# Performance work log

Measured on AMD Instinct MI355X. Metric: run time of the kernel, lower is better.

The kernel has to match this reference:

```python
import jax, jax.numpy as jnp
import numpy as np

N_HEADS = 32
N_KV_HEADS = 8
HEAD_DIM = 64
ROPE_THETA = 10000.0
NEG_INF = -1e9


def apply_rope(t, offset=0):
    # t: [B, H, L, hd]; half-split (rotate-half) RoPE convention
    B, H, L, hd = t.shape
    pos = jnp.arange(offset, offset + L, dtype=jnp.float32)            # [L]
    inv_freq = 1.0 / (ROPE_THETA ** (jnp.arange(0, hd, 2, dtype=jnp.float32) / hd))  # [hd/2]
    ang = pos[:, None] * inv_freq[None, :]                              # [L, hd/2]
    cos = jnp.cos(ang).astype(t.dtype)
    sin = jnp.sin(ang).astype(t.dtype)
    t1, t2 = jnp.split(t, 2, axis=-1)                                   # each [B,H,L,hd/2]
    return jnp.concatenate([t1 * cos - t2 * sin, t1 * sin + t2 * cos], axis=-1)


def setup_inputs() -> dict:
    key = jax.random.key(0)
    ks = jax.random.split(key, 6)
    B, L, D = 1, 2048, 2048
    x = jax.random.normal(ks[0], (B, L, D), dtype=jnp.float32)
    attn_scale = jnp.ones((1,), dtype=jnp.float32)
    # causal additive mask: 0 on/below diagonal, -1e9 above
    mask = jnp.where(jnp.tril(jnp.ones((L, L), dtype=bool)), 0.0, NEG_INF).astype(jnp.float32)
    s = 0.02
    Wq = jax.random.normal(ks[1], (N_HEADS * HEAD_DIM, D), dtype=jnp.float32) * s
    Wk = jax.random.normal(ks[2], (N_KV_HEADS * HEAD_DIM, D), dtype=jnp.float32) * s
    Wv = jax.random.normal(ks[3], (N_KV_HEADS * HEAD_DIM, D), dtype=jnp.float32) * s
    Wo = jax.random.normal(ks[4], (D, N_HEADS * HEAD_DIM), dtype=jnp.float32) * s
    return {"x": x, "attn_scale": attn_scale, "mask": mask,
            "Wq": Wq, "Wk": Wk, "Wv": Wv, "Wo": Wo}


def reference(x, attn_scale, mask, Wq, Wk, Wv, Wo):
    B, L, D = x.shape
    scale = HEAD_DIM ** -0.5
    # projections (nn.Linear: y = x @ W.T)
    q = (x @ Wq.T).reshape(B, L, N_HEADS, HEAD_DIM).transpose(0, 2, 1, 3)     # [B,H,L,hd]
    k = (x @ Wk.T).reshape(B, L, N_KV_HEADS, HEAD_DIM).transpose(0, 2, 1, 3)  # [B,Hk,L,hd]
    v = (x @ Wv.T).reshape(B, L, N_KV_HEADS, HEAD_DIM).transpose(0, 2, 1, 3)
    q = apply_rope(q)
    k = apply_rope(k)
    q = q * attn_scale  # elementwise attn_scale applied to queries
    # GQA: repeat kv heads
    rep = N_HEADS // N_KV_HEADS
    k = jnp.repeat(k, rep, axis=1)
    v = jnp.repeat(v, rep, axis=1)
    scores = jnp.einsum('bhld,bhmd->bhlm', q, k) * scale + mask
    probs = jax.nn.softmax(scores, axis=-1)
    out = jnp.einsum('bhlm,bhmd->bhld', probs, v)          # [B,H,L,hd]
    out = out.transpose(0, 2, 1, 3).reshape(B, L, N_HEADS * HEAD_DIM)
    return out @ Wo.T
```

## Files before the change

kernel.cpp:

```cpp
#include <hip/hip_runtime.h>
#include <stdint.h>

typedef short bf16x8 __attribute__((ext_vector_type(8)));
typedef float f32x4 __attribute__((ext_vector_type(4)));

__device__ __forceinline__ unsigned short f2bf(float f) {
  uint32_t u = __float_as_uint(f);
  u = (u + 0x7FFFu + ((u >> 16) & 1u)) >> 16;
  return (unsigned short)u;
}

__device__ __forceinline__ void gload16(const void* g, void* lds) {
  const __attribute__((address_space(1))) char* gp =
      (const __attribute__((address_space(1))) char*)(uintptr_t)g;
  __attribute__((address_space(3))) char* sp =
      (__attribute__((address_space(3))) char*)(uint32_t)(uintptr_t)lds;
  __builtin_amdgcn_global_load_lds(gp, sp, 16, 0, 0);
}

__global__ void k_cvt_all(const float* __restrict__ x, const float* __restrict__ Wq,
                          const float* __restrict__ Wk, const float* __restrict__ Wv,
                          const float* __restrict__ Wo, unsigned short* __restrict__ xb,
                          unsigned short* __restrict__ Wcat, unsigned short* __restrict__ Wob) {
  int b = blockIdx.x;
  const float* src;
  unsigned short* dst;
  int off;
  if (b < 4096)       { src = x;  dst = xb;                  off = b; }
  else if (b < 8192)  { src = Wq; dst = Wcat;                off = b - 4096; }
  else if (b < 9216)  { src = Wk; dst = Wcat + 2048 * 2048;  off = b - 8192; }
  else if (b < 10240) { src = Wv; dst = Wcat + 2560 * 2048;  off = b - 9216; }
  else                { src = Wo; dst = Wob;                  off = b - 10240; }
  int i = off * 256 + threadIdx.x;
  float4 v = ((const float4*)src)[i];
  ushort4 o;
  o.x = f2bf(v.x); o.y = f2bf(v.y); o.z = f2bf(v.z); o.w = f2bf(v.w);
  ((ushort4*)dst)[i] = o;
}

template <int OUTF32, int ROPE>
__global__ __launch_bounds__(256) void k_gemm(const unsigned short* __restrict__ A,
                                              const unsigned short* __restrict__ B,
                                              void* __restrict__ Cout,
                                              int M, int N, int K,
                                              const float* __restrict__ scale_p,
                                              unsigned short* __restrict__ vtout) {
  __shared__ unsigned short As[2][64 * 64];
  __shared__ unsigned short Bs[2][128 * 64];
  const int tid = threadIdx.x;
  const int w = tid >> 6, lane = tid & 63;
  const int g = lane >> 4, cl = lane & 15;
  const int nTn = N >> 7;
  const int per = gridDim.x >> 3;
  const int bid = (blockIdx.x & 7) * per + (blockIdx.x >> 3);
  const int tm = bid / nTn, tn = bid % nTn;
  const int m0 = tm << 6, n0 = tn << 7;
  const int wm = (w >> 1) << 5, wn = (w & 1) << 6;
  f32x4 acc[2][4] = {};

  auto stage = [&](int kt, int b) {
#pragma unroll
    for (int it = 0; it < 6; ++it) {
      int cc = tid + it * 256;
      int isB = cc >= 512;
      int c3 = isB ? (cc - 512) : cc;
      int row = c3 >> 3, kb = (c3 & 7) << 4;
      const unsigned short* base = isB ? (B + (size_t)(n0 + row) * K + kt)
                                       : (A + (size_t)(m0 + row) * K + kt);
      const char* src = (const char*)base + (kb ^ ((row & 7) << 4));
      char* dstl = (char*)(isB ? Bs[b] : As[b]) + c3 * 16;
      gload16(src, dstl);
    }
  };

  stage(0, 0);
  asm volatile("s_waitcnt vmcnt(0)" ::: "memory");
  __syncthreads();
  int buf = 0;

  for (int kt = 0; kt < K; kt += 64) {
    if (kt + 64 < K) stage(kt + 64, buf ^ 1);
#pragma unroll
    for (int ks = 0; ks < 2; ++ks) {
      bf16x8 af[2], bfr[4];
#pragma unroll
      for (int i = 0; i < 2; ++i) {
        int row = wm + i * 16 + cl;
        int kb = ((g << 4) + (ks << 6)) ^ ((row & 7) << 4);
        af[i] = *(const bf16x8*)((const char*)As[buf] + row * 128 + kb);
      }
#pragma unroll
      for (int j = 0; j < 4; ++j) {
        int row = wn + j * 16 + cl;
        int kb = ((g << 4) + (ks << 6)) ^ ((row & 7) << 4);
        bfr[j] = *(const bf16x8*)((const char*)Bs[buf] + row * 128 + kb);
      }
#pragma unroll
      for (int i = 0; i < 2; ++i)
#pragma unroll
        for (int j = 0; j < 4; ++j)
          acc[i][j] = __builtin_amdgcn_mfma_f32_16x16x32_bf16(af[i], bfr[j], acc[i][j], 0, 0, 0);
    }
    asm volatile("s_waitcnt vmcnt(0)" ::: "memory");
    __syncthreads();
    buf ^= 1;
  }

  if (ROPE && n0 >= 2560) {
#pragma unroll
    for (int i = 0; i < 2; ++i)
#pragma unroll
      for (int j = 0; j < 4; ++j) {
        int d = n0 - 2560 + wn + j * 16 + cl;
        int l0r = m0 + wm + i * 16 + (g << 2);
        ushort4 o;
        o.x = f2bf(acc[i][j][0]); o.y = f2bf(acc[i][j][1]);
        o.z = f2bf(acc[i][j][2]); o.w = f2bf(acc[i][j][3]);
        *(ushort4*)(vtout + (size_t)d * 2048 + l0r) = o;
      }
    return;
  }

  if (ROPE) {
    float s0v = scale_p[0] * 0.125f * 1.4426950408889634f;
    float sc = (n0 < 2048) ? s0v : 1.0f;
    float invf[2];
#pragma unroll
    for (int j = 0; j < 2; ++j)
      invf[j] = __expf(-(float)(j * 16 + cl) * 0.2878231366242557f);
#pragma unroll
    for (int i = 0; i < 2; ++i)
#pragma unroll
      for (int r = 0; r < 4; ++r) {
        float pos = (float)(m0 + wm + i * 16 + (g << 2) + r);
#pragma unroll
        for (int j = 0; j < 2; ++j) {
          float ang = pos * invf[j];
          float sn, cs;
          __sincosf(ang, &sn, &cs);
          float t1 = acc[i][j][r], t2 = acc[i][j + 2][r];
          acc[i][j][r] = (t1 * cs - t2 * sn) * sc;
          acc[i][j + 2][r] = (t1 * sn + t2 * cs) * sc;
        }
      }
  }

#pragma unroll
  for (int i = 0; i < 2; ++i)
#pragma unroll
    for (int j = 0; j < 4; ++j)
#pragma unroll
      for (int r = 0; r < 4; ++r) {
        int row = m0 + wm + i * 16 + (g << 2) + r;
        int col = n0 + wn + j * 16 + cl;
        float v = acc[i][j][r];
        if (OUTF32)
          ((float*)Cout)[(size_t)row * N + col] = v;
        else
          ((unsigned short*)Cout)[(size_t)row * N + col] = f2bf(v);
      }
}

__global__ __launch_bounds__(256) void k_attn(const unsigned short* __restrict__ qkv,
                                              const unsigned short* __restrict__ vt,
                                              unsigned short* __restrict__ ao) {
  __shared__ unsigned short Ks[2][64 * 64];
  __shared__ unsigned short Vs[2][64 * 64];
  __shared__ unsigned short Ps[4 * 16 * 64];
  const int tid = threadIdx.x;
  const int w = tid >> 6, lane = tid & 63;
  const int g = lane >> 4, cl = lane & 15;
  const int h = blockIdx.x & 31;
  const int qb = 31 - (blockIdx.x >> 5);
  const int q0 = qb << 6;
  const int hk = h >> 2;
  const int qg = q0 + w * 16 + cl;

  const unsigned short* qptr = qkv + (size_t)qg * 3072 + h * 64 + g * 8;
  bf16x8 qf0 = *(const bf16x8*)qptr;
  bf16x8 qf1 = *(const bf16x8*)(qptr + 32);

  const short ob = (short)0x3F80;
  const bf16x8 onesf = {ob, ob, ob, ob, ob, ob, ob, ob};

  f32x4 acc[4] = {};
  f32x4 acc_l = {};

  char* myP = (char*)Ps + w * 2048;

  int kvOff[2][4];
#pragma unroll
  for (int ks = 0; ks < 2; ++ks)
#pragma unroll
    for (int t = 0; t < 4; ++t) {
      int row = t * 16 + cl;
      kvOff[ks][t] = row * 128 + (((g << 4) + (ks << 6)) ^ ((row & 7) << 4));
    }
  int pwOff[4];
#pragma unroll
  for (int t = 0; t < 4; ++t)
    pwOff[t] = cl * 128 + (((t << 5) + (g << 3)) ^ ((cl & 7) << 4));
  int prOff[2];
#pragma unroll
  for (int ks = 0; ks < 2; ++ks)
    prOff[ks] = cl * 128 + (((g << 4) + (ks << 6)) ^ ((cl & 7) << 4));

  const int row0 = tid >> 3, row1 = (tid + 256) >> 3;
  const int kb0 = (tid & 7) << 4, kb1 = ((tid + 256) & 7) << 4;
  const char* kSrc0 = (const char*)(qkv + 2048 + hk * 64 + (size_t)row0 * 3072) + (kb0 ^ ((row0 & 7) << 4));
  const char* kSrc1 = (const char*)(qkv + 2048 + hk * 64 + (size_t)row1 * 3072) + (kb1 ^ ((row1 & 7) << 4));
  const char* vSrc0 = (const char*)(vt + (size_t)hk * 64 * 2048 + (size_t)row0 * 2048) + (kb0 ^ ((row0 & 7) << 4));
  const char* vSrc1 = (const char*)(vt + (size_t)hk * 64 * 2048 + (size_t)row1 * 2048) + (kb1 ^ ((row1 & 7) << 4));

  auto stageK = [&](int ck, int b) {
    size_t off = (size_t)ck * 393216;
    gload16(kSrc0 + off, (char*)Ks[b] + tid * 16);
    gload16(kSrc1 + off, (char*)Ks[b] + (tid + 256) * 16);
  };
  auto stageV = [&](int ck, int b) {
    size_t off = (size_t)ck * 128;
    gload16(vSrc0 + off, (char*)Vs[b] + tid * 16);
    gload16(vSrc1 + off, (char*)Vs[b] + (tid + 256) * 16);
  };

  stageK(0, 0); stageV(0, 0);
  if (qb >= 1) stageK(1, 1);
  asm volatile("s_waitcnt vmcnt(0)" ::: "memory");
  __syncthreads();

  float svA[4][4], svB[4][4];
  {
    const char* Kc = (const char*)Ks[0];
    __builtin_amdgcn_s_setprio(1);
#pragma unroll
    for (int t = 0; t < 4; ++t) {
      f32x4 stv = {};
#pragma unroll
      for (int ks = 0; ks < 2; ++ks) {
        bf16x8 kf = *(const bf16x8*)(Kc + kvOff[ks][t]);
        stv = __builtin_amdgcn_mfma_f32_16x16x32_bf16(kf, ks ? qf1 : qf0, stv, 0, 0, 0);
      }
#pragma unroll
      for (int r = 0; r < 4; ++r) svA[t][r] = stv[r];
    }
    __builtin_amdgcn_s_setprio(0);
  }
  __syncthreads();

#define ATTN_BODY(I, CUR, NXT)                                                         \
  {                                                                                    \
    const int i_ = (I);                                                                \
    if (i_ + 2 <= qb) stageK(i_ + 2, i_ & 1);                                          \
    if (i_ + 1 <= qb) stageV(i_ + 1, (i_ + 1) & 1);                                    \
    if (i_ < qb) {                                                                     \
      const char* Kc = (const char*)Ks[(i_ + 1) & 1];                                  \
      __builtin_amdgcn_s_setprio(1);                                                   \
      _Pragma("unroll")                                                                \
      for (int t = 0; t < 4; ++t) {                                                    \
        f32x4 stv = {};                                                                \
        _Pragma("unroll")                                                              \
        for (int ks = 0; ks < 2; ++ks) {                                               \
          bf16x8 kf = *(const bf16x8*)(Kc + kvOff[ks][t]);                             \
          stv = __builtin_amdgcn_mfma_f32_16x16x32_bf16(kf, ks ? qf1 : qf0, stv, 0, 0, 0); \
        }                                                                              \
        _Pragma("unroll")                                                              \
        for (int r = 0; r < 4; ++r) NXT[t][r] = stv[r];                                \
      }                                                                                \
      __builtin_amdgcn_s_setprio(0);                                                   \
    }                                                                                  \
    if (i_ == qb) {                                                                    \
      const int kv0 = i_ << 6;                                                         \
      _Pragma("unroll")                                                                \
      for (int t = 0; t < 4; ++t)                                                      \
        _Pragma("unroll")                                                              \
        for (int r = 0; r < 4; ++r) {                                                  \
          int kvg = kv0 + t * 16 + (g << 2) + r;                                       \
          if (kvg > qg) CUR[t][r] = -1e9f;                                             \
        }                                                                              \
    }                                                                                  \
    _Pragma("unroll")                                                                  \
    for (int t = 0; t < 4; ++t) {                                                      \
      float e0 = __builtin_exp2f(CUR[t][0]);                                           \
      float e1 = __builtin_exp2f(CUR[t][1]);                                           \
      float e2 = __builtin_exp2f(CUR[t][2]);                                           \
      float e3 = __builtin_exp2f(CUR[t][3]);                                           \
      uint32_t d0, d1;                                                                 \
      asm("v_cvt_pk_bf16_f32 %0, %1, %2" : "=v"(d0) : "v"(e0), "v"(e1));               \
      asm("v_cvt_pk_bf16_f32 %0, %1, %2" : "=v"(d1) : "v"(e2), "v"(e3));               \
      uint2 dd; dd.x = d0; dd.y = d1;                                                  \
      *(uint2*)(myP + pwOff[t]) = dd;                                                  \
    }                                                                                  \
    {                                                                                  \
      const char* Vc = (const char*)Vs[i_ & 1];                                        \
      __builtin_amdgcn_s_setprio(1);                                                   \
      _Pragma("unroll")                                                                \
      for (int ks = 0; ks < 2; ++ks) {                                                 \
        bf16x8 pf = *(const bf16x8*)(myP + prOff[ks]);                                 \
        acc_l = __builtin_amdgcn_mfma_f32_16x16x32_bf16(pf, onesf, acc_l, 0, 0, 0);    \
        _Pragma("unroll")                                                              \
        for (int t = 0; t < 4; ++t) {                                                  \
          bf16x8 vf = *(const bf16x8*)(Vc + kvOff[ks][t]);                             \
          acc[t] = __builtin_amdgcn_mfma_f32_16x16x32_bf16(pf, vf, acc[t], 0, 0, 0);   \
        }                                                                              \
      }                                                                                \
      __builtin_amdgcn_s_setprio(0);                                                   \
    }                                                                                  \
    if (i_ < qb) {                                                                     \
      asm volatile("s_waitcnt vmcnt(0)" ::: "memory");                                 \
      __syncthreads();                                                                 \
    }                                                                                  \
  }

  for (int i = 0; i <= qb; i += 2) {
    ATTN_BODY(i, svA, svB);
    if (i + 1 <= qb) ATTN_BODY(i + 1, svB, svA);
  }
#undef ATTN_BODY

  float li[4];
#pragma unroll
  for (int r = 0; r < 4; ++r) li[r] = 1.0f / acc_l[r];
#pragma unroll
  for (int t = 0; t < 4; ++t)
#pragma unroll
    for (int r = 0; r < 4; ++r) {
      int row = q0 + w * 16 + (g << 2) + r;
      int col = h * 64 + t * 16 + cl;
      ao[(size_t)row * 2048 + col] = f2bf(acc[t][r] * li[r]);
    }
}

extern "C" void kernel_launch(void* const* d_in, const int* in_sizes, int n_in,
                              void* d_out, int out_size, void* d_ws, size_t ws_size,
                              hipStream_t stream) {
  (void)in_sizes; (void)n_in; (void)out_size; (void)ws_size;
  const float* x  = (const float*)d_in[0];
  const float* sc = (const float*)d_in[1];
  const float* Wq = (const float*)d_in[3];
  const float* Wk = (const float*)d_in[4];
  const float* Wv = (const float*)d_in[5];
  const float* Wo = (const float*)d_in[6];
  float* out = (float*)d_out;
  char* ws = (char*)d_ws;
  unsigned short* xb   = (unsigned short*)(ws);
  unsigned short* Wcat = (unsigned short*)(ws + 8388608);
  unsigned short* Wob  = (unsigned short*)(ws + 20971520);
  unsigned short* QKV  = (unsigned short*)(ws + 29360128);
  unsigned short* VT   = (unsigned short*)(ws + 41943040);
  unsigned short* AO   = (unsigned short*)(ws + 44040192);

  k_cvt_all<<<14336, 256, 0, stream>>>(x, Wq, Wk, Wv, Wo, xb, Wcat, Wob);
  k_gemm<0, 1><<<768, 256, 0, stream>>>(xb, Wcat, QKV, 2048, 3072, 2048, sc, VT);
  k_attn<<<1024, 256, 0, stream>>>(QKV, VT, AO);
  k_gemm<1, 0><<<512, 256, 0, stream>>>(AO, Wob, out, 2048, 2048, 2048, nullptr, nullptr);
}
```

Measured before the change: 116.1 us.

## Fuse attention and output projection into one persistent launch with per-row-block counters

The attention kernel and the output-projection GEMM are merged into one launch of 1536 blocks. Output-GEMM blocks spin on per-query-block completion counters, so each row tile starts once all 32 heads for that row block are written, overlapping the projection with the attention tail. The output GEMM also changes from the K=64 tiling to a K=32 tiling with its own swizzle. This saves a kernel launch and the tail idle time, at the cost of a memset, spin-waiting blocks that hold CU slots, and a deadlock risk if GEMM blocks get scheduled before attention blocks finish.

```diff
diff --git a/kernel.cpp b/kernel.cpp
--- a/kernel.cpp
+++ b/kernel.cpp
@@ -38,13 +38,12 @@
   ((ushort4*)dst)[i] = o;
 }
 
-template <int OUTF32, int ROPE>
-__global__ __launch_bounds__(256) void k_gemm(const unsigned short* __restrict__ A,
-                                              const unsigned short* __restrict__ B,
-                                              void* __restrict__ Cout,
-                                              int M, int N, int K,
-                                              const float* __restrict__ scale_p,
-                                              unsigned short* __restrict__ vtout) {
+__global__ __launch_bounds__(256) void k_gemm0(const unsigned short* __restrict__ A,
+                                               const unsigned short* __restrict__ B,
+                                               unsigned short* __restrict__ Cout,
+                                               const float* __restrict__ scale_p,
+                                               unsigned short* __restrict__ vtout) {
+  const int K = 2048, N = 3072;
   __shared__ unsigned short As[2][64 * 64];
   __shared__ unsigned short Bs[2][128 * 64];
   const int tid = threadIdx.x;
@@ -106,7 +105,7 @@
     buf ^= 1;
   }
 
-  if (ROPE && n0 >= 2560) {
+  if (n0 >= 2560) {
 #pragma unroll
     for (int i = 0; i < 2; ++i)
 #pragma unroll
@@ -121,7 +120,7 @@
     return;
   }
 
-  if (ROPE) {
+  {
     float s0v = scale_p[0] * 0.125f * 1.4426950408889634f;
     float sc = (n0 < 2048) ? s0v : 1.0f;
     float invf[2];
@@ -153,181 +152,257 @@
       for (int r = 0; r < 4; ++r) {
         int row = m0 + wm + i * 16 + (g << 2) + r;
         int col = n0 + wn + j * 16 + cl;
-        float v = acc[i][j][r];
-        if (OUTF32)
-          ((float*)Cout)[(size_t)row * N + col] = v;
-        else
-          ((unsigned short*)Cout)[(size_t)row * N + col] = f2bf(v);
-      }
-}
-
-__global__ __launch_bounds__(256) void k_attn(const unsigned short* __restrict__ qkv,
-                                              const unsigned short* __restrict__ vt,
-                                              unsigned short* __restrict__ ao) {
-  __shared__ unsigned short Ks[2][64 * 64];
-  __shared__ unsigned short Vs[2][64 * 64];
-  __shared__ unsigned short Ps[4 * 16 * 64];
+        Cout[(size_t)row * N + col] = f2bf(acc[i][j][r]);
+      }
+}
+
+__global__ __launch_bounds__(256) void k_attn_g1(const unsigned short* __restrict__ qkv,
+                                                 const unsigned short* __restrict__ vt,
+                                                 unsigned short* __restrict__ ao,
+                                                 const unsigned short* __restrict__ Wob,
+                                                 float* __restrict__ out,
+                                                 int* __restrict__ done) {
+  __shared__ __align__(16) char smem[40960];
   const int tid = threadIdx.x;
   const int w = tid >> 6, lane = tid & 63;
   const int g = lane >> 4, cl = lane & 15;
-  const int h = blockIdx.x & 31;
-  const int qb = 31 - (blockIdx.x >> 5);
-  const int q0 = qb << 6;
-  const int hk = h >> 2;
-  const int qg = q0 + w * 16 + cl;
-
-  const unsigned short* qptr = qkv + (size_t)qg * 3072 + h * 64 + g * 8;
-  bf16x8 qf0 = *(const bf16x8*)qptr;
-  bf16x8 qf1 = *(const bf16x8*)(qptr + 32);
-
-  const short ob = (short)0x3F80;
-  const bf16x8 onesf = {ob, ob, ob, ob, ob, ob, ob, ob};
-
-  f32x4 acc[4] = {};
-  f32x4 acc_l = {};
-
-  char* myP = (char*)Ps + w * 2048;
-
-  int kvOff[2][4];
-#pragma unroll
-  for (int ks = 0; ks < 2; ++ks)
-#pragma unroll
-    for (int t = 0; t < 4; ++t) {
-      int row = t * 16 + cl;
-      kvOff[ks][t] = row * 128 + (((g << 4) + (ks << 6)) ^ ((row & 7) << 4));
-    }
-  int pwOff[4];
-#pragma unroll
-  for (int t = 0; t < 4; ++t)
-    pwOff[t] = cl * 128 + (((t << 5) + (g << 3)) ^ ((cl & 7) << 4));
-  int prOff[2];
-#pragma unroll
-  for (int ks = 0; ks < 2; ++ks)
-    prOff[ks] = cl * 128 + (((g << 4) + (ks << 6)) ^ ((cl & 7) << 4));
-
-  const int row0 = tid >> 3, row1 = (tid + 256) >> 3;
-  const int kb0 = (tid & 7) << 4, kb1 = ((tid + 256) & 7) << 4;
-  const char* kSrc0 = (const char*)(qkv + 2048 + hk * 64 + (size_t)row0 * 3072) + (kb0 ^ ((row0 & 7) << 4));
-  const char* kSrc1 = (const char*)(qkv + 2048 + hk * 64 + (size_t)row1 * 3072) + (kb1 ^ ((row1 & 7) << 4));
-  const char* vSrc0 = (const char*)(vt + (size_t)hk * 64 * 2048 + (size_t)row0 * 2048) + (kb0 ^ ((row0 & 7) << 4));
-  const char* vSrc1 = (const char*)(vt + (size_t)hk * 64 * 2048 + (size_t)row1 * 2048) + (kb1 ^ ((row1 & 7) << 4));
-
-  auto stageK = [&](int ck, int b) {
-    size_t off = (size_t)ck * 393216;
-    gload16(kSrc0 + off, (char*)Ks[b] + tid * 16);
-    gload16(kSrc1 + off, (char*)Ks[b] + (tid + 256) * 16);
-  };
-  auto stageV = [&](int ck, int b) {
-    size_t off = (size_t)ck * 128;
-    gload16(vSrc0 + off, (char*)Vs[b] + tid * 16);
-    gload16(vSrc1 + off, (char*)Vs[b] + (tid + 256) * 16);
-  };
-
-  stageK(0, 0); stageV(0, 0);
-  if (qb >= 1) stageK(1, 1);
-  asm volatile("s_waitcnt vmcnt(0)" ::: "memory");
-  __syncthreads();
-
-  float svA[4][4], svB[4][4];
-  {
-    const char* Kc = (const char*)Ks[0];
-    __builtin_amdgcn_s_setprio(1);
-#pragma unroll
-    for (int t = 0; t < 4; ++t) {
-      f32x4 stv = {};
-#pragma unroll
-      for (int ks = 0; ks < 2; ++ks) {
-        bf16x8 kf = *(const bf16x8*)(Kc + kvOff[ks][t]);
-        stv = __builtin_amdgcn_mfma_f32_16x16x32_bf16(kf, ks ? qf1 : qf0, stv, 0, 0, 0);
-      }
-#pragma unroll
-      for (int r = 0; r < 4; ++r) svA[t][r] = stv[r];
-    }
-    __builtin_amdgcn_s_setprio(0);
-  }
-  __syncthreads();
+
+  if (blockIdx.x < 1024) {
+    unsigned short (*Ks)[64 * 64] = (unsigned short (*)[64 * 64])smem;
+    unsigned short (*Vs)[64 * 64] = (unsigned short (*)[64 * 64])(smem + 16384);
+    char* Ps = smem + 32768;
+    const int h = blockIdx.x & 31;
+    const int qb = 31 - (blockIdx.x >> 5);
+    const int q0 = qb << 6;
+    const int hk = h >> 2;
+    const int qg = q0 + w * 16 + cl;
+
+    const unsigned short* qptr = qkv + (size_t)qg * 3072 + h * 64 + g * 8;
+    bf16x8 qf0 = *(const bf16x8*)qptr;
+    bf16x8 qf1 = *(const bf16x8*)(qptr + 32);
+
+    const short ob = (short)0x3F80;
+    const bf16x8 onesf = {ob, ob, ob, ob, ob, ob, ob, ob};
+
+    f32x4 acc[4] = {};
+    f32x4 acc_l = {};
+
+    char* myP = Ps + w * 2048;
+
+    int kvOff[2][4];
+#pragma unroll
+    for (int ks = 0; ks < 2; ++ks)
+#pragma unroll
+      for (int t = 0; t < 4; ++t) {
+        int row = t * 16 + cl;
+        kvOff[ks][t] = row * 128 + (((g << 4) + (ks << 6)) ^ ((row & 7) << 4));
+      }
+    int pwOff[4];
+#pragma unroll
+    for (int t = 0; t < 4; ++t)
+      pwOff[t] = cl * 128 + (((t << 5) + (g << 3)) ^ ((cl & 7) << 4));
+    int prOff[2];
+#pragma unroll
+    for (int ks = 0; ks < 2; ++ks)
+      prOff[ks] = cl * 128 + (((g << 4) + (ks << 6)) ^ ((cl & 7) << 4));
+
+    const int row0 = tid >> 3, row1 = (tid + 256) >> 3;
+    const int kb0 = (tid & 7) << 4, kb1 = ((tid + 256) & 7) << 4;
+    const char* kSrc0 = (const char*)(qkv + 2048 + hk * 64 + (size_t)row0 * 3072) + (kb0 ^ ((row0 & 7) << 4));
+    const char* kSrc1 = (const char*)(qkv + 2048 + hk * 64 + (size_t)row1 * 3072) + (kb1 ^ ((row1 & 7) << 4));
+    const char* vSrc0 = (const char*)(vt + (size_t)hk * 64 * 2048 + (size_t)row0 * 2048) + (kb0 ^ ((row0 & 7) << 4));
+    const char* vSrc1 = (const char*)(vt + (size_t)hk * 64 * 2048 + (size_t)row1 * 2048) + (kb1 ^ ((row1 & 7) << 4));
+
+    auto stageK = [&](int ck, int b) {
+      size_t off = (size_t)ck * 393216;
+      gload16(kSrc0 + off, (char*)Ks[b] + tid * 16);
+      gload16(kSrc1 + off, (char*)Ks[b] + (tid + 256) * 16);
+    };
+    auto stageV = [&](int ck, int b) {
+      size_t off = (size_t)ck * 128;
+      gload16(vSrc0 + off, (char*)Vs[b] + tid * 16);
+      gload16(vSrc1 + off, (char*)Vs[b] + (tid + 256) * 16);
+    };
+
+    stageK(0, 0); stageV(0, 0);
+    if (qb >= 1) stageK(1, 1);
+    asm volatile("s_waitcnt vmcnt(0)" ::: "memory");
+    __syncthreads();
+
+    float svA[4][4], svB[4][4];
+    {
+      const char* Kc = (const char*)Ks[0];
+      __builtin_amdgcn_s_setprio(1);
+#pragma unroll
+      for (int t = 0; t < 4; ++t) {
+        f32x4 stv = {};
+#pragma unroll
+        for (int ks = 0; ks < 2; ++ks) {
+          bf16x8 kf = *(const bf16x8*)(Kc + kvOff[ks][t]);
+          stv = __builtin_amdgcn_mfma_f32_16x16x32_bf16(kf, ks ? qf1 : qf0, stv, 0, 0, 0);
+        }
+#pragma unroll
+        for (int r = 0; r < 4; ++r) svA[t][r] = stv[r];
+      }
+      __builtin_amdgcn_s_setprio(0);
+    }
+    __syncthreads();
 
 #define ATTN_BODY(I, CUR, NXT)                                                         \
-  {                                                                                    \
-    const int i_ = (I);                                                                \
-    if (i_ + 2 <= qb) stageK(i_ + 2, i_ & 1);                                          \
-    if (i_ + 1 <= qb) stageV(i_ + 1, (i_ + 1) & 1);                                    \
-    if (i_ < qb) {                                                                     \
-      const char* Kc = (const char*)Ks[(i_ + 1) & 1];                                  \
-      __builtin_amdgcn_s_setprio(1);                                                   \
+    {                                                                                  \
+      const int i_ = (I);                                                              \
+      if (i_ + 2 <= qb) stageK(i_ + 2, i_ & 1);                                        \
+      if (i_ + 1 <= qb) stageV(i_ + 1, (i_ + 1) & 1);                                  \
+      if (i_ < qb) {                                                                   \
+        const char* Kc = (const char*)Ks[(i_ + 1) & 1];                                \
+        __builtin_amdgcn_s_setprio(1);                                                 \
+        _Pragma("unroll")                                                              \
+        for (int t = 0; t < 4; ++t) {                                                  \
+          f32x4 stv = {};                                                              \
+          _Pragma("unroll")                                                            \
+          for (int ks = 0; ks < 2; ++ks) {                                             \
+            bf16x8 kf = *(const bf16x8*)(Kc + kvOff[ks][t]);                           \
+            stv = __builtin_amdgcn_mfma_f32_16x16x32_bf16(kf, ks ? qf1 : qf0, stv, 0, 0, 0); \
+          }                                                                            \
+          _Pragma("unroll")                                                            \
+          for (int r = 0; r < 4; ++r) NXT[t][r] = stv[r];                              \
+        }                                                                              \
+        __builtin_amdgcn_s_setprio(0);                                                 \
+      }                                                                                \
+      if (i_ == qb) {                                                                  \
+        const int kv0 = i_ << 6;                                                       \
+        _Pragma("unroll")                                                              \
+        for (int t = 0; t < 4; ++t)                                                    \
+          _Pragma("unroll")                                                            \
+          for (int r = 0; r < 4; ++r) {                                                \
+            int kvg = kv0 + t * 16 + (g << 2) + r;                                     \
+            if (kvg > qg) CUR[t][r] = -1e9f;                                           \
+          }                                                                            \
+      }                                                                                \
       _Pragma("unroll")                                                                \
       for (int t = 0; t < 4; ++t) {                                                    \
-        f32x4 stv = {};                                                                \
+        float e0 = __builtin_exp2f(CUR[t][0]);                                         \
+        float e1 = __builtin_exp2f(CUR[t][1]);                                         \
+        float e2 = __builtin_exp2f(CUR[t][2]);                                         \
+        float e3 = __builtin_exp2f(CUR[t][3]);                                         \
+        uint32_t d0, d1;                                                               \
+        asm("v_cvt_pk_bf16_f32 %0, %1, %2" : "=v"(d0) : "v"(e0), "v"(e1));             \
+        asm("v_cvt_pk_bf16_f32 %0, %1, %2" : "=v"(d1) : "v"(e2), "v"(e3));             \
+        uint2 dd; dd.x = d0; dd.y = d1;                                                \
+        *(uint2*)(myP + pwOff[t]) = dd;                                                \
+      }                                                                                \
+      {                                                                                \
+        const char* Vc = (const char*)Vs[i_ & 1];                                      \
+        __builtin_amdgcn_s_setprio(1);                                                 \
         _Pragma("unroll")                                                              \
         for (int ks = 0; ks < 2; ++ks) {                                               \
-          bf16x8 kf = *(const bf16x8*)(Kc + kvOff[ks][t]);                             \
-          stv = __builtin_amdgcn_mfma_f32_16x16x32_bf16(kf, ks ? qf1 : qf0, stv, 0, 0, 0); \
+          bf16x8 pf = *(const bf16x8*)(myP + prOff[ks]);                               \
+          acc_l = __builtin_amdgcn_mfma_f32_16x16x32_bf16(pf, onesf, acc_l, 0, 0, 0);  \
+          _Pragma("unroll")                                                            \
+          for (int t = 0; t < 4; ++t) {                                                \
+            bf16x8 vf = *(const bf16x8*)(Vc + kvOff[ks][t]);                           \
+            acc[t] = __builtin_amdgcn_mfma_f32_16x16x32_bf16(pf, vf, acc[t], 0, 0, 0); \
+          }                                                                            \
         }                                                                              \
-        _Pragma("unroll")                                                              \
-        for (int r = 0; r < 4; ++r) NXT[t][r] = stv[r];                                \
+        __builtin_amdgcn_s_setprio(0);                                                 \
       }                                                                                \
-      __builtin_amdgcn_s_setprio(0);                                                   \
-    }                                                                                  \
-    if (i_ == qb) {                                                                    \
-      const int kv0 = i_ << 6;                                                         \
-      _Pragma("unroll")                                                                \
-      for (int t = 0; t < 4; ++t)                                                      \
-        _Pragma("unroll")                                                              \
-        for (int r = 0; r < 4; ++r) {                                                  \
-          int kvg = kv0 + t * 16 + (g << 2) + r;                                       \
-          if (kvg > qg) CUR[t][r] = -1e9f;                                             \
-        }                                                                              \
-    }                                                                                  \
-    _Pragma("unroll")                                                                  \
-    for (int t = 0; t < 4; ++t) {                                                      \
-      float e0 = __builtin_exp2f(CUR[t][0]);                                           \
-      float e1 = __builtin_exp2f(CUR[t][1]);                                           \
-      float e2 = __builtin_exp2f(CUR[t][2]);                                           \
-      float e3 = __builtin_exp2f(CUR[t][3]);                                           \
-      uint32_t d0, d1;                                                                 \
-      asm("v_cvt_pk_bf16_f32 %0, %1, %2" : "=v"(d0) : "v"(e0), "v"(e1));               \
-      asm("v_cvt_pk_bf16_f32 %0, %1, %2" : "=v"(d1) : "v"(e2), "v"(e3));               \
-      uint2 dd; dd.x = d0; dd.y = d1;                                                  \
-      *(uint2*)(myP + pwOff[t]) = dd;                                                  \
-    }                                                                                  \
-    {                                                                                  \
-      const char* Vc = (const char*)Vs[i_ & 1];                                        \
-      __builtin_amdgcn_s_setprio(1);                                                   \
-      _Pragma("unroll")                                                                \
-      for (int ks = 0; ks < 2; ++ks) {                                                 \
-        bf16x8 pf = *(const bf16x8*)(myP + prOff[ks]);                                 \
-        acc_l = __builtin_amdgcn_mfma_f32_16x16x32_bf16(pf, onesf, acc_l, 0, 0, 0);    \
-        _Pragma("unroll")                                                              \
-        for (int t = 0; t < 4; ++t) {                                                  \
-          bf16x8 vf = *(const bf16x8*)(Vc + kvOff[ks][t]);                             \
-          acc[t] = __builtin_amdgcn_mfma_f32_16x16x32_bf16(pf, vf, acc[t], 0, 0, 0);   \
-        }                                                                              \
+      if (i_ < qb) {                                                                   \
+        asm volatile("s_waitcnt vmcnt(0)" ::: "memory");                               \
+        __syncthreads();                                                               \
       }                                                                                \
-      __builtin_amdgcn_s_setprio(0);                                                   \
-    }                                                                                  \
-    if (i_ < qb) {                                                                     \
-      asm volatile("s_waitcnt vmcnt(0)" ::: "memory");                                 \
-      __syncthreads();                                                                 \
-    }                                                                                  \
+    }
+
+    for (int i = 0; i <= qb; i += 2) {
+      ATTN_BODY(i, svA, svB);
+      if (i + 1 <= qb) ATTN_BODY(i + 1, svB, svA);
+    }
+#undef ATTN_BODY
+
+    float li[4];
+#pragma unroll
+    for (int r = 0; r < 4; ++r) li[r] = 1.0f / acc_l[r];
+#pragma unroll
+    for (int t = 0; t < 4; ++t)
+#pragma unroll
+      for (int r = 0; r < 4; ++r) {
+        int row = q0 + w * 16 + (g << 2) + r;
+        int col = h * 64 + t * 16 + cl;
+        ao[(size_t)row * 2048 + col] = f2bf(acc[t][r] * li[r]);
+      }
+
+    __threadfence();
+    __syncthreads();
+    if (tid == 0) atomicAdd(&done[qb], 1);
+  } else {
+    unsigned short* As0 = (unsigned short*)smem;
+    unsigned short* Bs0 = (unsigned short*)(smem + 8192);
+    const int ib = blockIdx.x - 1024;
+    const int bid = (ib & 7) * 64 + (ib >> 3);
+    const int tm = bid >> 4, tn = bid & 15;
+    const int m0 = tm << 6, n0 = tn << 7;
+    const int wm = (w >> 1) << 5, wn = (w & 1) << 6;
+
+    if (tid == 0) {
+      while (__hip_atomic_load(&done[tm], __ATOMIC_RELAXED, __HIP_MEMORY_SCOPE_AGENT) < 32)
+        __builtin_amdgcn_s_sleep(32);
+    }
+    __syncthreads();
+    __threadfence();
+
+    f32x4 acc[2][4] = {};
+    auto stage = [&](int kt, int b) {
+#pragma unroll
+      for (int it = 0; it < 3; ++it) {
+        int cc = tid + it * 256;
+        int isB = cc >= 256;
+        int c3 = isB ? (cc - 256) : cc;
+        int row = c3 >> 2, kb = (c3 & 3) << 4;
+        const unsigned short* base = isB ? (Wob + (size_t)(n0 + row) * 2048 + kt)
+                                         : (ao + (size_t)(m0 + row) * 2048 + kt);
+        const char* src = (const char*)base + (kb ^ ((row & 3) << 4));
+        char* dstl = (char*)(isB ? (Bs0 + b * 4096) : (As0 + b * 2048)) + c3 * 16;
+        gload16(src, dstl);
+      }
+    };
+
+    stage(0, 0);
+    asm volatile("s_waitcnt vmcnt(0)" ::: "memory");
+    __syncthreads();
+    int buf = 0;
+
+    for (int kt = 0; kt < 2048; kt += 32) {
+      if (kt + 32 < 2048) stage(kt + 32, buf ^ 1);
+      bf16x8 af[2], bfr[4];
+#pragma unroll
+      for (int i = 0; i < 2; ++i) {
+        int row = wm + i * 16 + cl;
+        af[i] = *(const bf16x8*)((const char*)(As0 + buf * 2048) + row * 64 + ((g << 4) ^ ((row & 3) << 4)));
+      }
+#pragma unroll
+      for (int j = 0; j < 4; ++j) {
+        int row = wn + j * 16 + cl;
+        bfr[j] = *(const bf16x8*)((const char*)(Bs0 + buf * 4096) + row * 64 + ((g << 4) ^ ((row & 3) << 4)));
+      }
+#pragma unroll
+      for (int i = 0; i < 2; ++i)
+#pragma unroll
+        for (int j = 0; j < 4; ++j)
+          acc[i][j] = __builtin_amdgcn_mfma_f32_16x16x32_bf16(af[i], bfr[j], acc[i][j], 0, 0, 0);
+      asm volatile("s_waitcnt vmcnt(0)" ::: "memory");
+      __syncthreads();
+      buf ^= 1;
+    }
+#pragma unroll
+    for (int i = 0; i < 2; ++i)
+#pragma unroll
+      for (int j = 0; j < 4; ++j)
+#pragma unroll
+        for (int r = 0; r < 4; ++r) {
+          int row = m0 + wm + i * 16 + (g << 2) + r;
+          int col = n0 + wn + j * 16 + cl;
+          out[(size_t)row * 2048 + col] = acc[i][j][r];
+        }
   }
-
-  for (int i = 0; i <= qb; i += 2) {
-    ATTN_BODY(i, svA, svB);
-    if (i + 1 <= qb) ATTN_BODY(i + 1, svB, svA);
-  }
-#undef ATTN_BODY
-
-  float li[4];
-#pragma unroll
-  for (int r = 0; r < 4; ++r) li[r] = 1.0f / acc_l[r];
-#pragma unroll
-  for (int t = 0; t < 4; ++t)
-#pragma unroll
-    for (int r = 0; r < 4; ++r) {
-      int row = q0 + w * 16 + (g << 2) + r;
-      int col = h * 64 + t * 16 + cl;
-      ao[(size_t)row * 2048 + col] = f2bf(acc[t][r] * li[r]);
-    }
 }
 
 extern "C" void kernel_launch(void* const* d_in, const int* in_sizes, int n_in,
@@ -348,9 +423,10 @@
   unsigned short* QKV  = (unsigned short*)(ws + 29360128);
   unsigned short* VT   = (unsigned short*)(ws + 41943040);
   unsigned short* AO   = (unsigned short*)(ws + 44040192);
-
+  int* done            = (int*)(ws + 52428800);
+
+  hipMemsetAsync(done, 0, 128, stream);
   k_cvt_all<<<14336, 256, 0, stream>>>(x, Wq, Wk, Wv, Wo, xb, Wcat, Wob);
-  k_gemm<0, 1><<<768, 256, 0, stream>>>(xb, Wcat, QKV, 2048, 3072, 2048, sc, VT);
-  k_attn<<<1024, 256, 0, stream>>>(QKV, VT, AO);
-  k_gemm<1, 0><<<512, 256, 0, stream>>>(AO, Wob, out, 2048, 2048, 2048, nullptr, nullptr);
-}
+  k_gemm0<<<768, 256, 0, stream>>>(xb, Wcat, QKV, sc, VT);
+  k_attn_g1<<<1536, 256, 0, stream>>>(QKV, VT, AO, Wob, out, done);
+}
```

Result: slower. 339.2 us (+192.1%).
